# Kernel optimization log

Hardware: AMD Instinct MI355X
Metric: run time of the kernel (lower is better)

The kernel has to match this reference:

```python
import jax, jax.numpy as jnp
import numpy as np

HID, H, D, DFF = 128, 4, 128, 2048   # hidden_dim, nheads, out_feats per head, dim_feedforward
N, E, B = 32768, 524288, 32
EPS = 1e-5
SLOPE = 0.2  # DGL EdgeGATConv negative_slope default


def setup_inputs() -> dict:
    key = jax.random.key(0)
    ks = jax.random.split(key, 16)
    s = 0.05
    return {
        "h": jax.random.normal(ks[0], (N, HID), jnp.float32),
        "e": jax.random.normal(ks[1], (E, 1), jnp.float32),
        "src": jax.random.randint(ks[2], (E,), 0, N, jnp.int32),
        "dst": jax.random.randint(ks[3], (E,), 0, N, jnp.int32),
        "batch_size": B,
        # EdgeGATConv params (fc / fc_edge / res_fc are bias-free in DGL)
        "W_fc": jax.random.normal(ks[4], (HID, H * D), jnp.float32) * s,
        "attn_l": jax.random.normal(ks[5], (H, D), jnp.float32) * s,
        "attn_r": jax.random.normal(ks[6], (H, D), jnp.float32) * s,
        "W_fe": jax.random.normal(ks[7], (1, H * D), jnp.float32) * s,
        "attn_e": jax.random.normal(ks[8], (H, D), jnp.float32) * s,
        "W_res": jax.random.normal(ks[9], (HID, H * D), jnp.float32) * s,
        "gat_bias": jnp.zeros((H * D,), jnp.float32),
        # linear_mha + norms + FFN
        "W_mha": jax.random.normal(ks[10], (H * D, HID), jnp.float32) * s,
        "b_mha": jnp.zeros((HID,), jnp.float32),
        "n1_g": jnp.ones((HID,), jnp.float32),
        "n1_b": jnp.zeros((HID,), jnp.float32),
        "n2_g": jnp.ones((HID,), jnp.float32),
        "n2_b": jnp.zeros((HID,), jnp.float32),
        "W1": jax.random.normal(ks[11], (HID, DFF), jnp.float32) * s,
        "b1": jnp.zeros((DFF,), jnp.float32),
        "W2": jax.random.normal(ks[12], (DFF, HID), jnp.float32) * s,
        "b2": jnp.zeros((HID,), jnp.float32),
    }


def _ln(x, g, b):
    mu = x.mean(-1, keepdims=True)
    var = ((x - mu) ** 2).mean(-1, keepdims=True)
    return (x - mu) * jax.lax.rsqrt(var + EPS) * g + b


def reference(h, e, src, dst, batch_size, W_fc, attn_l, attn_r, W_fe, attn_e,
              W_res, gat_bias, W_mha, b_mha, n1_g, n1_b, n2_g, n2_b,
              W1, b1, W2, b2):
    n = h.shape[0]
    h0 = h
    # --- EdgeGATConv (eval mode: dropouts are identity) ---
    ft = (h @ W_fc).reshape(n, H, D)                         # (N,H,D)
    el = jnp.einsum("nhd,hd->nh", ft, attn_l)                # (N,H)
    er = jnp.einsum("nhd,hd->nh", ft, attn_r)
    fe = (e @ W_fe).reshape(-1, H, D)                        # (E,H,D)
    ee = jnp.einsum("ehd,hd->eh", fe, attn_e)                # (E,H)
    sc = jax.nn.leaky_relu(el[src] + er[dst] + ee, SLOPE)    # (E,H)
    # segment softmax over incoming edges of each dst node
    m = jax.ops.segment_max(sc, dst, num_segments=n)         # (N,H)
    m = jnp.where(jnp.isfinite(m), m, 0.0)                   # empty segments
    w = jnp.exp(sc - m[dst])
    z = jax.ops.segment_sum(w, dst, num_segments=n)
    zd = z[dst]
    alpha = w / jnp.where(zd == 0, 1.0, zd)                  # (E,H)
    msg = ft[src] * alpha[:, :, None]                        # (E,H,D)
    rst = jax.ops.segment_sum(msg, dst, num_segments=n)      # (N,H,D)
    rst = rst + (h0 @ W_res).reshape(n, H, D) + gat_bias.reshape(1, H, D)
    # --- transformer wrapper ---
    x = jax.nn.relu(rst).reshape(n, H * D)
    x = jax.nn.relu(x @ W_mha + b_mha)
    x = _ln(h0 + x, n1_g, n1_b)
    x = x.reshape(batch_size, -1, x.shape[1])                # (B, N/B, HID)
    ff = jax.nn.relu(x @ W1 + b1) @ W2 + b2
    return _ln(x + ff, n2_g, n2_b)
```

## Files before the change

kernel.cpp:

```cpp
#include <hip/hip_runtime.h>
#include <hip/hip_bf16.h>

#define N_NODES 32768
#define E_EDGES 524288
#define HIDDIM 128
#define FDIM 512
#define DFF 2048
#define LN_EPS 1e-5f
#define SLOPE 0.2f
#define CAP 64

typedef __bf16 bf16_t;
typedef __bf16 bf16x8 __attribute__((ext_vector_type(8)));
typedef float f32x4 __attribute__((ext_vector_type(4)));
typedef float f32x2 __attribute__((ext_vector_type(2)));

#define GLD_LDS16(gp, lp) __builtin_amdgcn_global_load_lds( \
    (const __attribute__((address_space(1))) unsigned int*)(gp), \
    (__attribute__((address_space(3))) unsigned int*)(lp), 16, 0, 0)

__device__ inline unsigned char f32_to_e4m3(float v) {
#if __has_builtin(__builtin_amdgcn_cvt_pk_fp8_f32)
    return (unsigned char)(__builtin_amdgcn_cvt_pk_fp8_f32(v, v, 0, false) & 0xff);
#else
    unsigned bits = __float_as_uint(v);
    unsigned sign = (bits >> 24) & 0x80;
    float av = fabsf(v);
    if (av >= 448.f) return (unsigned char)(sign | 0x7E);
    int e = (int)((bits >> 23) & 0xFF) - 127;
    if (e < -6) { int n = (int)rintf(av * 512.f); return (unsigned char)(sign | n); }
    float ulp = exp2f((float)(e - 3));
    int n = (int)rintf(av / ulp);
    if (n == 16) { e += 1; n = 8; }
    return (unsigned char)(sign | ((e + 7) << 3) | (n - 8));
#endif
}
template<bool HI>
__device__ inline f32x2 e4m3x2_to_f32(unsigned u) {
#if __has_builtin(__builtin_amdgcn_cvt_pk_f32_fp8)
    return __builtin_amdgcn_cvt_pk_f32_fp8(u, HI);
#else
    f32x2 r;
    unsigned b0 = HI ? ((u >> 16) & 0xff) : (u & 0xff);
    unsigned b1 = HI ? ((u >> 24) & 0xff) : ((u >> 8) & 0xff);
    unsigned bs[2] = {b0, b1};
    for (int i = 0; i < 2; ++i) {
        unsigned b = bs[i];
        float s = (b & 0x80) ? -1.f : 1.f;
        int e = (b >> 3) & 15, m = b & 7;
        float v = e ? (8 + m) * exp2f((float)(e - 10)) : m * exp2f(-9.f);
        r[i] = s * v;
    }
    return r;
#endif
}

__device__ inline void pack_range(const float* __restrict__ B, bf16_t* __restrict__ out,
                                  int id, int N) {
    const int g = id / N, n = id % N;
    union { bf16_t b[8]; uint4 u; } pk;
#pragma unroll
    for (int j = 0; j < 8; ++j) pk.b[j] = (bf16_t)B[(size_t)(g * 8 + j) * N + n];
    *(uint4*)(out + (size_t)id * 8) = pk.u;
}

__global__ __launch_bounds__(256) void prep_kernel(const float* __restrict__ h, bf16_t* __restrict__ hb,
                                                   const float* __restrict__ W_fc, bf16_t* __restrict__ Wfc_p,
                                                   const float* __restrict__ W_res, bf16_t* __restrict__ Wres_p,
                                                   const float* __restrict__ W_mha, bf16_t* __restrict__ Wmha_p,
                                                   const float* __restrict__ W1, bf16_t* __restrict__ W1_p,
                                                   const float* __restrict__ W2, bf16_t* __restrict__ W2_p,
                                                   const float* __restrict__ W_fe, const float* __restrict__ attn_e,
                                                   float* __restrict__ ce) {
    int bid = blockIdx.x;
    const int tid = threadIdx.x;
    if (bid < 4096) {
        const int id = bid * 256 + tid;
        const float4 v = ((const float4*)h)[id];
        union { bf16_t b[4]; uint2 u; } pk;
        pk.b[0] = (bf16_t)v.x; pk.b[1] = (bf16_t)v.y; pk.b[2] = (bf16_t)v.z; pk.b[3] = (bf16_t)v.w;
        *(uint2*)(hb + (size_t)id * 4) = pk.u;
        return;
    }
    bid -= 4096;
    if (bid < 32)  { pack_range(W_fc,  Wfc_p,  bid * 256 + tid, 512);  return; }
    bid -= 32;
    if (bid < 32)  { pack_range(W_res, Wres_p, bid * 256 + tid, 512);  return; }
    bid -= 32;
    if (bid < 32)  { pack_range(W_mha, Wmha_p, bid * 256 + tid, 128);  return; }
    bid -= 32;
    if (bid < 128) { pack_range(W1,    W1_p,   bid * 256 + tid, 2048); return; }
    bid -= 128;
    if (bid < 128) { pack_range(W2,    W2_p,   bid * 256 + tid, 128);  return; }
    if (tid < 128) {
        const float4 w = ((const float4*)W_fe)[tid];
        const float4 a = ((const float4*)attn_e)[tid];
        float p = w.x * a.x + w.y * a.y + w.z * a.z + w.w * a.w;
        for (int off = 16; off; off >>= 1) p += __shfl_down(p, off, 32);
        if ((tid & 31) == 0) ce[tid >> 5] = p;
    }
}

__global__ __launch_bounds__(256) void gemm_mfma(const bf16_t* __restrict__ A,
                                                 const bf16_t* __restrict__ Bp,
                                                 bf16_t* __restrict__ C,
                                                 int M, int N, int K) {
    __shared__ __align__(16) bf16_t lA[4096];
    __shared__ __align__(16) bf16_t lB[4096];
    const int tid = threadIdx.x;
    const int lane = tid & 63;
    const int wave = tid >> 6;
    const int wm = (wave >> 1) * 64, wn = (wave & 1) * 64;
    const int row0 = blockIdx.y * 128, col0 = blockIdx.x * 128;
    const int ko = lane >> 4;
    const int rl = lane & 15;
    f32x4 acc[4][4] = {};
    const int c0 = tid, c1 = tid + 256;
    const int g0 = c0 >> 7, m0 = c0 & 127;
    const int g1 = c1 >> 7, m1 = c1 & 127;
    for (int k0 = 0; k0 < K; k0 += 32) {
        __syncthreads();
        GLD_LDS16(A + (size_t)(row0 + m0) * K + k0 + g0 * 8, lA + c0 * 8);
        GLD_LDS16(A + (size_t)(row0 + m1) * K + k0 + g1 * 8, lA + c1 * 8);
        GLD_LDS16(Bp + ((size_t)(k0 / 8 + g0) * N + col0 + m0) * 8, lB + c0 * 8);
        GLD_LDS16(Bp + ((size_t)(k0 / 8 + g1) * N + col0 + m1) * 8, lB + c1 * 8);
        __syncthreads();
        bf16x8 af[4], bfr[4];
#pragma unroll
        for (int i = 0; i < 4; ++i) {
            af[i]  = *(const bf16x8*)&lA[(ko * 128 + wm + i * 16 + rl) * 8];
            bfr[i] = *(const bf16x8*)&lB[(ko * 128 + wn + i * 16 + rl) * 8];
        }
#pragma unroll
        for (int i = 0; i < 4; ++i)
#pragma unroll
            for (int j = 0; j < 4; ++j)
                acc[i][j] = __builtin_amdgcn_mfma_f32_16x16x32_bf16(af[i], bfr[j], acc[i][j], 0, 0, 0);
    }
    const int cr = (lane >> 4) * 4;
    const int cc = lane & 15;
#pragma unroll
    for (int i = 0; i < 4; ++i)
#pragma unroll
        for (int j = 0; j < 4; ++j) {
            const int col = col0 + wn + j * 16 + cc;
#pragma unroll
            for (int r = 0; r < 4; ++r) {
                const int row = row0 + wm + i * 16 + cr + r;
                C[(size_t)row * N + col] = (bf16_t)acc[i][j][r];
            }
        }
}

__global__ __launch_bounds__(256) void gemm_ft(const bf16_t* __restrict__ A,
                                               const bf16_t* __restrict__ Bp,
                                               const float* __restrict__ attn_l,
                                               const float* __restrict__ attn_r,
                                               unsigned char* __restrict__ ft8,
                                               float* __restrict__ el,
                                               float* __restrict__ er) {
    __shared__ __align__(16) bf16_t lA[4096];
    __shared__ __align__(16) bf16_t lB[4096];
    __shared__ float s_el[2][128], s_er[2][128];
    const int tid = threadIdx.x, lane = tid & 63, wave = tid >> 6;
    const int wm = (wave >> 1) * 64, wn = (wave & 1) * 64;
    const int row0 = blockIdx.y * 128;
    const int head = blockIdx.x, col0 = head * 128;
    const int ko = lane >> 4, rl = lane & 15;
    f32x4 acc[4][4] = {};
    const int c0 = tid, c1 = tid + 256;
    const int g0 = c0 >> 7, m0 = c0 & 127;
    const int g1 = c1 >> 7, m1 = c1 & 127;
    for (int k0 = 0; k0 < 128; k0 += 32) {
        __syncthreads();
        GLD_LDS16(A + (size_t)(row0 + m0) * 128 + k0 + g0 * 8, lA + c0 * 8);
        GLD_LDS16(A + (size_t)(row0 + m1) * 128 + k0 + g1 * 8, lA + c1 * 8);
        GLD_LDS16(Bp + ((size_t)(k0 / 8 + g0) * 512 + col0 + m0) * 8, lB + c0 * 8);
        GLD_LDS16(Bp + ((size_t)(k0 / 8 + g1) * 512 + col0 + m1) * 8, lB + c1 * 8);
        __syncthreads();
        bf16x8 af[4], bfr[4];
#pragma unroll
        for (int i = 0; i < 4; ++i) {
            af[i]  = *(const bf16x8*)&lA[(ko * 128 + wm + i * 16 + rl) * 8];
            bfr[i] = *(const bf16x8*)&lB[(ko * 128 + wn + i * 16 + rl) * 8];
        }
#pragma unroll
        for (int i = 0; i < 4; ++i)
#pragma unroll
            for (int j = 0; j < 4; ++j)
                acc[i][j] = __builtin_amdgcn_mfma_f32_16x16x32_bf16(af[i], bfr[j], acc[i][j], 0, 0, 0);
    }
    const int cr = (lane >> 4) * 4, cc = lane & 15;
    float al[4], ar[4];
#pragma unroll
    for (int j = 0; j < 4; ++j) {
        al[j] = attn_l[col0 + wn + j * 16 + cc];
        ar[j] = attn_r[col0 + wn + j * 16 + cc];
    }
#pragma unroll
    for (int i = 0; i < 4; ++i)
#pragma unroll
        for (int r = 0; r < 4; ++r) {
            const int row = row0 + wm + i * 16 + cr + r;
            float pel = 0.f, per = 0.f;
#pragma unroll
            for (int j = 0; j < 4; ++j) {
                const float v = acc[i][j][r];
                ft8[(size_t)row * 512 + col0 + wn + j * 16 + cc] = f32_to_e4m3(v);
                pel += v * al[j];
                per += v * ar[j];
            }
#pragma unroll
            for (int m = 1; m < 16; m <<= 1) {
                pel += __shfl_xor(pel, m);
                per += __shfl_xor(per, m);
            }
            if (cc == 0) {
                s_el[wn >> 6][wm + i * 16 + cr + r] = pel;
                s_er[wn >> 6][wm + i * 16 + cr + r] = per;
            }
        }
    __syncthreads();
    if (tid < 128) {
        el[(size_t)(row0 + tid) * 4 + head] = s_el[0][tid] + s_el[1][tid];
        er[(size_t)(row0 + tid) * 4 + head] = s_er[0][tid] + s_er[1][tid];
    }
}

__global__ __launch_bounds__(256) void gemm_mha_ln(const bf16_t* __restrict__ A,
                                                   const bf16_t* __restrict__ Bp,
                                                   const float* __restrict__ bias,
                                                   const float* __restrict__ h0,
                                                   const float* __restrict__ gamma,
                                                   const float* __restrict__ beta,
                                                   bf16_t* __restrict__ out) {
    __shared__ __align__(16) bf16_t lA[4096];
    __shared__ __align__(16) bf16_t lB[4096];
    __shared__ float s_s1[2][128], s_s2[2][128], s_mu[128], s_rs[128];
    const int tid = threadIdx.x, lane = tid & 63, wave = tid >> 6;
    const int wm = (wave >> 1) * 64, wn = (wave & 1) * 64;
    const int row0 = blockIdx.x * 128;
    const int ko = lane >> 4, rl = lane & 15;
    f32x4 acc[4][4] = {};
    const int c0 = tid, c1 = tid + 256;
    const int g0 = c0 >> 7, m0 = c0 & 127;
    const int g1 = c1 >> 7, m1 = c1 & 127;
    for (int k0 = 0; k0 < 512; k0 += 32) {
        __syncthreads();
        GLD_LDS16(A + (size_t)(row0 + m0) * 512 + k0 + g0 * 8, lA + c0 * 8);
        GLD_LDS16(A + (size_t)(row0 + m1) * 512 + k0 + g1 * 8, lA + c1 * 8);
        GLD_LDS16(Bp + ((size_t)(k0 / 8 + g0) * 128 + m0) * 8, lB + c0 * 8);
        GLD_LDS16(Bp + ((size_t)(k0 / 8 + g1) * 128 + m1) * 8, lB + c1 * 8);
        __syncthreads();
        bf16x8 af[4], bfr[4];
#pragma unroll
        for (int i = 0; i < 4; ++i) {
            af[i]  = *(const bf16x8*)&lA[(ko * 128 + wm + i * 16 + rl) * 8];
            bfr[i] = *(const bf16x8*)&lB[(ko * 128 + wn + i * 16 + rl) * 8];
        }
#pragma unroll
        for (int i = 0; i < 4; ++i)
#pragma unroll
            for (int j = 0; j < 4; ++j)
                acc[i][j] = __builtin_amdgcn_mfma_f32_16x16x32_bf16(af[i], bfr[j], acc[i][j], 0, 0, 0);
    }
    const int cr = (lane >> 4) * 4, cc = lane & 15;
#pragma unroll
    for (int j = 0; j < 4; ++j) {
        const int col = wn + j * 16 + cc;
        const float bb = bias[col];
#pragma unroll
        for (int i = 0; i < 4; ++i)
#pragma unroll
            for (int r = 0; r < 4; ++r) {
                const int row = row0 + wm + i * 16 + cr + r;
                acc[i][j][r] = fmaxf(acc[i][j][r] + bb, 0.f) + h0[(size_t)row * 128 + col];
            }
    }
#pragma unroll
    for (int i = 0; i < 4; ++i)
#pragma unroll
        for (int r = 0; r < 4; ++r) {
            float s1 = 0.f, s2 = 0.f;
#pragma unroll
            for (int j = 0; j < 4; ++j) { const float v = acc[i][j][r]; s1 += v; s2 += v * v; }
#pragma unroll
            for (int m = 1; m < 16; m <<= 1) {
                s1 += __shfl_xor(s1, m);
                s2 += __shfl_xor(s2, m);
            }
            if (cc == 0) {
                s_s1[wn >> 6][wm + i * 16 + cr + r] = s1;
                s_s2[wn >> 6][wm + i * 16 + cr + r] = s2;
            }
        }
    __syncthreads();
    if (tid < 128) {
        const float a = s_s1[0][tid] + s_s1[1][tid];
        const float q = s_s2[0][tid] + s_s2[1][tid];
        const float mu = a * (1.f / 128.f);
        s_mu[tid] = mu;
        s_rs[tid] = rsqrtf(q * (1.f / 128.f) - mu * mu + LN_EPS);
    }
    __syncthreads();
#pragma unroll
    for (int j = 0; j < 4; ++j) {
        const int col = wn + j * 16 + cc;
        const float gg = gamma[col], bb = beta[col];
#pragma unroll
        for (int i = 0; i < 4; ++i)
#pragma unroll
            for (int r = 0; r < 4; ++r) {
                const int rloc = wm + i * 16 + cr + r;
                out[(size_t)(row0 + rloc) * 128 + col] =
                    (bf16_t)((acc[i][j][r] - s_mu[rloc]) * s_rs[rloc] * gg + bb);
            }
    }
}

__global__ __launch_bounds__(256, 1) void ffn_fused(const bf16_t* __restrict__ x3,
                                                    const bf16_t* __restrict__ W1p,
                                                    const float* __restrict__ b1,
                                                    const bf16_t* __restrict__ W2p,
                                                    const float* __restrict__ b2,
                                                    const float* __restrict__ gamma,
                                                    const float* __restrict__ beta,
                                                    float* __restrict__ out) {
    __shared__ __align__(16) bf16_t lX[16384];
    __shared__ __align__(16) bf16_t lW1[2][8192];
    __shared__ __align__(16) bf16_t lW2[2][8192];
    __shared__ __align__(16) bf16_t lY[8192];
    __shared__ float s_s1[2][128], s_s2[2][128], s_mu[128], s_rs[128];
    const int tid = threadIdx.x, lane = tid & 63, wave = tid >> 6;
    const int wm = (wave >> 1) * 64;
    const int wn1 = (wave & 1) * 32;
    const int wn2 = (wave & 1) * 64;
    const int row0 = blockIdx.x * 128;
    const int ko = lane >> 4, rl = lane & 15;
    const int cr = ko * 4, cc = rl;

#pragma unroll
    for (int it = 0; it < 8; ++it) {
        const int c = it * 256 + tid, g = c >> 7, m = c & 127;
        GLD_LDS16(x3 + (size_t)(row0 + m) * 128 + g * 8, lX + c * 8);
    }
#pragma unroll
    for (int it = 0; it < 4; ++it) {
        const int c = it * 256 + tid;
        { const int g = c >> 6, n = c & 63;  GLD_LDS16(W1p + ((size_t)g * 2048 + n) * 8, lW1[0] + c * 8); }
        { const int g = c >> 7, n = c & 127; GLD_LDS16(W2p + ((size_t)g * 128 + n) * 8, lW2[0] + c * 8); }
    }
    __syncthreads();
    bf16x8 afx[4][4];
#pragma unroll
    for (int i = 0; i < 4; ++i)
#pragma unroll
        for (int kk = 0; kk < 4; ++kk)
            afx[i][kk] = *(const bf16x8*)&lX[((kk * 4 + ko) * 128 + wm + i * 16 + rl) * 8];

    f32x4 xacc[4][4] = {};
    for (int ch = 0; ch < 32; ++ch) {
        const int b = ch & 1;
        f32x4 yacc[4][2] = {};
#pragma unroll
        for (int kk = 0; kk < 4; ++kk) {
            bf16x8 bfr[2];
#pragma unroll
            for (int j = 0; j < 2; ++j)
                bfr[j] = *(const bf16x8*)&lW1[b][((kk * 4 + ko) * 64 + wn1 + j * 16 + rl) * 8];
#pragma unroll
            for (int i = 0; i < 4; ++i)
#pragma unroll
                for (int j = 0; j < 2; ++j)
                    yacc[i][j] = __builtin_amdgcn_mfma_f32_16x16x32_bf16(afx[i][kk], bfr[j], yacc[i][j], 0, 0, 0);
        }
#pragma unroll
        for (int j = 0; j < 2; ++j) {
            const int dff = wn1 + j * 16 + cc;
            const float bb = b1[ch * 64 + dff];
#pragma unroll
            for (int i = 0; i < 4; ++i)
#pragma unroll
                for (int r = 0; r < 4; ++r)
                    lY[((dff >> 3) * 128 + wm + i * 16 + cr + r) * 8 + (dff & 7)] =
                        (bf16_t)fmaxf(yacc[i][j][r] + bb, 0.f);
        }
        __syncthreads();
        if (ch + 1 < 32) {
            const int nb = b ^ 1, nch = ch + 1;
#pragma unroll
            for (int it = 0; it < 4; ++it) {
                const int c = it * 256 + tid;
                { const int g = c >> 6, n = c & 63;  GLD_LDS16(W1p + ((size_t)g * 2048 + nch * 64 + n) * 8, lW1[nb] + c * 8); }
                { const int g = c >> 7, n = c & 127; GLD_LDS16(W2p + ((size_t)(nch * 8 + g) * 128 + n) * 8, lW2[nb] + c * 8); }
            }
        }
#pragma unroll
        for (int kk = 0; kk < 2; ++kk) {
            bf16x8 afY[4], bfr2[4];
#pragma unroll
            for (int i = 0; i < 4; ++i)
                afY[i] = *(const bf16x8*)&lY[((kk * 4 + ko) * 128 + wm + i * 16 + rl) * 8];
#pragma unroll
            for (int j = 0; j < 4; ++j)
                bfr2[j] = *(const bf16x8*)&lW2[b][((kk * 4 + ko) * 128 + wn2 + j * 16 + rl) * 8];
#pragma unroll
            for (int i = 0; i < 4; ++i)
#pragma unroll
                for (int j = 0; j < 4; ++j)
                    xacc[i][j] = __builtin_amdgcn_mfma_f32_16x16x32_bf16(afY[i], bfr2[j], xacc[i][j], 0, 0, 0);
        }
        __syncthreads();
    }
#pragma unroll
    for (int j = 0; j < 4; ++j) {
        const int col = wn2 + j * 16 + cc;
        const float bb = b2[col];
#pragma unroll
        for (int i = 0; i < 4; ++i)
#pragma unroll
            for (int r = 0; r < 4; ++r) {
                const int rloc = wm + i * 16 + cr + r;
                const float x3v = (float)lX[((col >> 3) * 128 + rloc) * 8 + (col & 7)];
                xacc[i][j][r] += bb + x3v;
            }
    }
#pragma unroll
    for (int i = 0; i < 4; ++i)
#pragma unroll
        for (int r = 0; r < 4; ++r) {
            float s1 = 0.f, s2 = 0.f;
#pragma unroll
            for (int j = 0; j < 4; ++j) { const float v = xacc[i][j][r]; s1 += v; s2 += v * v; }
#pragma unroll
            for (int m = 1; m < 16; m <<= 1) {
                s1 += __shfl_xor(s1, m);
                s2 += __shfl_xor(s2, m);
            }
            if (cc == 0) {
                s_s1[wn2 >> 6][wm + i * 16 + cr + r] = s1;
                s_s2[wn2 >> 6][wm + i * 16 + cr + r] = s2;
            }
        }
    __syncthreads();
    if (tid < 128) {
        const float a = s_s1[0][tid] + s_s1[1][tid];
        const float q = s_s2[0][tid] + s_s2[1][tid];
        const float mu = a * (1.f / 128.f);
        s_mu[tid] = mu;
        s_rs[tid] = rsqrtf(q * (1.f / 128.f) - mu * mu + LN_EPS);
    }
    __syncthreads();
#pragma unroll
    for (int j = 0; j < 4; ++j) {
        const int col = wn2 + j * 16 + cc;
        const float gg = gamma[col], bb = beta[col];
#pragma unroll
        for (int i = 0; i < 4; ++i)
#pragma unroll
            for (int r = 0; r < 4; ++r) {
                const int rloc = wm + i * 16 + cr + r;
                out[(size_t)(row0 + rloc) * 128 + col] =
                    (xacc[i][j][r] - s_mu[rloc]) * s_rs[rloc] * gg + bb;
            }
    }
}

__global__ __launch_bounds__(256) void edge_build(const float* __restrict__ evals,
                                                  const int* __restrict__ src,
                                                  const int* __restrict__ dst,
                                                  const float* __restrict__ el,
                                                  const float* __restrict__ er,
                                                  const float* __restrict__ ce,
                                                  int* __restrict__ cursor,
                                                  int* __restrict__ csr_src,
                                                  float4* __restrict__ csr_w) {
    const int e = blockIdx.x * 256 + threadIdx.x;
    const int s = src[e], d = dst[e];
    const float ev = evals[e];
    const float4 l = *(const float4*)(el + (size_t)s * 4);
    const float4 r = *(const float4*)(er + (size_t)d * 4);
    const float4 c = *(const float4*)ce;
    float4 w;
    {
        float v;
        v = l.x + r.x + ev * c.x; v = v >= 0.f ? v : SLOPE * v; w.x = __expf(v);
        v = l.y + r.y + ev * c.y; v = v >= 0.f ? v : SLOPE * v; w.y = __expf(v);
        v = l.z + r.z + ev * c.z; v = v >= 0.f ? v : SLOPE * v; w.z = __expf(v);
        v = l.w + r.w + ev * c.w; v = v >= 0.f ? v : SLOPE * v; w.w = __expf(v);
    }
    const int pos = atomicAdd(&cursor[d], 1);
    if (pos < CAP) {
        csr_src[(size_t)d * CAP + pos] = s;
        csr_w[(size_t)d * CAP + pos] = w;
    }
}

__global__ __launch_bounds__(128) void aggregate_kernel(const unsigned char* __restrict__ ft8,
                                                        const bf16_t* __restrict__ res,
                                                        const int* __restrict__ cursor,
                                                        const int* __restrict__ csr_src,
                                                        const float4* __restrict__ csr_w,
                                                        const float* __restrict__ gat_bias,
                                                        bf16_t* __restrict__ x1) {
    const int n = blockIdx.x, t = threadIdx.x;
    __shared__ int s_src[CAP];
    __shared__ float s_w[CAP][4];
    const int deg = min(cursor[n], CAP);
    const int ht = t >> 5;
    if (t < deg) {
        s_src[t] = csr_src[(size_t)n * CAP + t];
        *(float4*)s_w[t] = csr_w[(size_t)n * CAP + t];
    }
    __syncthreads();
    float4 acc = {0.f, 0.f, 0.f, 0.f};
    float z = 0.f;
    for (int j = 0; j < deg; ++j) {
        const float w = s_w[j][ht];
        z += w;
        const unsigned u = *(const unsigned*)(ft8 + (size_t)s_src[j] * 512 + t * 4);
        const f32x2 lo = e4m3x2_to_f32<false>(u);
        const f32x2 hi = e4m3x2_to_f32<true>(u);
        acc.x += w * lo[0]; acc.y += w * lo[1];
        acc.z += w * hi[0]; acc.w += w * hi[1];
    }
    const float rz = deg > 0 ? 1.f / z : 0.f;
    const uint2 ur = *(const uint2*)(res + (size_t)n * FDIM + t * 4);
    const float4 gb = ((const float4*)gat_bias)[t];
    union { bf16_t b[4]; uint2 u; } pk;
    pk.b[0] = (bf16_t)fmaxf(acc.x * rz + __uint_as_float(ur.x << 16) + gb.x, 0.f);
    pk.b[1] = (bf16_t)fmaxf(acc.y * rz + __uint_as_float(ur.x & 0xFFFF0000u) + gb.y, 0.f);
    pk.b[2] = (bf16_t)fmaxf(acc.z * rz + __uint_as_float(ur.y << 16) + gb.z, 0.f);
    pk.b[3] = (bf16_t)fmaxf(acc.w * rz + __uint_as_float(ur.y & 0xFFFF0000u) + gb.w, 0.f);
    *(uint2*)(x1 + (size_t)n * FDIM + t * 4) = pk.u;
}

extern "C" void kernel_launch(void* const* d_in, const int* in_sizes, int n_in,
                              void* d_out, int out_size, void* d_ws, size_t ws_size,
                              hipStream_t stream) {
    const float* h        = (const float*)d_in[0];
    const float* evals    = (const float*)d_in[1];
    const int*   src      = (const int*)d_in[2];
    const int*   dst      = (const int*)d_in[3];
    const float* W_fc     = (const float*)d_in[5];
    const float* attn_l   = (const float*)d_in[6];
    const float* attn_r   = (const float*)d_in[7];
    const float* W_fe     = (const float*)d_in[8];
    const float* attn_e   = (const float*)d_in[9];
    const float* W_res    = (const float*)d_in[10];
    const float* gat_bias = (const float*)d_in[11];
    const float* W_mha    = (const float*)d_in[12];
    const float* b_mha    = (const float*)d_in[13];
    const float* n1_g     = (const float*)d_in[14];
    const float* n1_b     = (const float*)d_in[15];
    const float* n2_g     = (const float*)d_in[16];
    const float* n2_b     = (const float*)d_in[17];
    const float* W1       = (const float*)d_in[18];
    const float* b1       = (const float*)d_in[19];
    const float* W2       = (const float*)d_in[20];
    const float* b2       = (const float*)d_in[21];

    char* ws = (char*)d_ws;
    unsigned char* ft8 = (unsigned char*)(ws + 0);
    bf16_t* res     = (bf16_t*)(ws + 16777216ull);
    bf16_t* x1      = (bf16_t*)(ws + 50331648ull);
    float4* csr_w   = (float4*)(ws + 83886080ull);
    int*    csr_src = (int*)   (ws + 117440512ull);
    bf16_t* x3b     = (bf16_t*)(ws + 125829120ull);
    bf16_t* hb      = (bf16_t*)(ws + 134217728ull);
    bf16_t* Wfc_p   = (bf16_t*)(ws + 142606336ull);
    bf16_t* Wres_p  = (bf16_t*)(ws + 142737408ull);
    bf16_t* Wmha_p  = (bf16_t*)(ws + 142868480ull);
    bf16_t* W1_p    = (bf16_t*)(ws + 142999552ull);
    bf16_t* W2_p    = (bf16_t*)(ws + 143523840ull);
    float*  el      = (float*) (ws + 144048128ull);
    float*  er      = (float*) (ws + 144572416ull);
    float*  ce      = (float*) (ws + 145096704ull);
    int*    cursor  = (int*)   (ws + 145096768ull);

    if (ws_size < 146000000ull) return;

    (void)hipMemsetAsync(cursor, 0, 131072, stream);

    prep_kernel<<<4449, 256, 0, stream>>>(h, hb, W_fc, Wfc_p, W_res, Wres_p,
                                          W_mha, Wmha_p, W1, W1_p, W2, W2_p,
                                          W_fe, attn_e, ce);
    gemm_ft<<<dim3(4, 256), 256, 0, stream>>>(hb, Wfc_p, attn_l, attn_r, ft8, el, er);
    gemm_mfma<<<dim3(4, 256), 256, 0, stream>>>(hb, Wres_p, res, N_NODES, FDIM, 128);
    edge_build<<<E_EDGES / 256, 256, 0, stream>>>(evals, src, dst, el, er, ce, cursor, csr_src, csr_w);
    aggregate_kernel<<<N_NODES, 128, 0, stream>>>(ft8, res, cursor, csr_src, csr_w, gat_bias, x1);
    gemm_mha_ln<<<256, 256, 0, stream>>>(x1, Wmha_p, b_mha, h, n1_g, n1_b, x3b);
    ffn_fused<<<256, 256, 0, stream>>>(x3b, W1_p, b1, W2_p, b2, n2_g, n2_b, (float*)d_out);
}
```

Baseline: 328.7 us.

## Halve FFN row tile to 64 and drop weight double-buffering for more blocks

The fused FFN kernel now processes 64 rows per block instead of 128, launching 512 blocks with launch bounds allowing two blocks per CU. The double-buffered W1/W2 LDS staging and the persistent X tile in LDS are removed, which shrinks LDS and register use. The aim is to fill all CUs (256 CUs with 512 blocks) and raise occupancy. In exchange, each weight chunk is loaded synchronously with no prefetch overlap, weight traffic per row doubles, and the residual is re-read from global memory.

Measured after the change: 297.7 us. 1.1x faster.

```diff
diff --git a/kernel.cpp b/kernel.cpp
--- a/kernel.cpp
+++ b/kernel.cpp
@@ -318,7 +318,7 @@
     }
 }
 
-__global__ __launch_bounds__(256, 1) void ffn_fused(const bf16_t* __restrict__ x3,
+__global__ __launch_bounds__(256, 2) void ffn_fused(const bf16_t* __restrict__ x3,
                                                     const bf16_t* __restrict__ W1p,
                                                     const float* __restrict__ b1,
                                                     const bf16_t* __restrict__ W2p,
@@ -326,107 +326,96 @@
                                                     const float* __restrict__ gamma,
                                                     const float* __restrict__ beta,
                                                     float* __restrict__ out) {
-    __shared__ __align__(16) bf16_t lX[16384];
-    __shared__ __align__(16) bf16_t lW1[2][8192];
-    __shared__ __align__(16) bf16_t lW2[2][8192];
-    __shared__ __align__(16) bf16_t lY[8192];
-    __shared__ float s_s1[2][128], s_s2[2][128], s_mu[128], s_rs[128];
+    __shared__ __align__(16) bf16_t lW1[8192];
+    __shared__ __align__(16) bf16_t lW2[8192];
+    __shared__ __align__(16) bf16_t lY[4096];
+    __shared__ float s_s1[2][64], s_s2[2][64], s_mu[64], s_rs[64];
     const int tid = threadIdx.x, lane = tid & 63, wave = tid >> 6;
-    const int wm = (wave >> 1) * 64;
-    const int wn1 = (wave & 1) * 32;
-    const int wn2 = (wave & 1) * 64;
-    const int row0 = blockIdx.x * 128;
+    const int wr  = (wave >> 1) * 32;
+    const int wc1 = (wave & 1) * 32;
+    const int wc2 = (wave & 1) * 64;
+    const int row0 = blockIdx.x * 64;
     const int ko = lane >> 4, rl = lane & 15;
     const int cr = ko * 4, cc = rl;
 
 #pragma unroll
-    for (int it = 0; it < 8; ++it) {
-        const int c = it * 256 + tid, g = c >> 7, m = c & 127;
-        GLD_LDS16(x3 + (size_t)(row0 + m) * 128 + g * 8, lX + c * 8);
-    }
-#pragma unroll
     for (int it = 0; it < 4; ++it) {
-        const int c = it * 256 + tid;
-        { const int g = c >> 6, n = c & 63;  GLD_LDS16(W1p + ((size_t)g * 2048 + n) * 8, lW1[0] + c * 8); }
-        { const int g = c >> 7, n = c & 127; GLD_LDS16(W2p + ((size_t)g * 128 + n) * 8, lW2[0] + c * 8); }
-    }
-    __syncthreads();
-    bf16x8 afx[4][4];
-#pragma unroll
-    for (int i = 0; i < 4; ++i)
+        const int c = it * 256 + tid, g = c >> 6, m = c & 63;
+        GLD_LDS16(x3 + (size_t)(row0 + m) * 128 + g * 8, lW1 + c * 8);
+    }
+    __syncthreads();
+    bf16x8 afx[2][4];
+#pragma unroll
+    for (int i = 0; i < 2; ++i)
 #pragma unroll
         for (int kk = 0; kk < 4; ++kk)
-            afx[i][kk] = *(const bf16x8*)&lX[((kk * 4 + ko) * 128 + wm + i * 16 + rl) * 8];
-
-    f32x4 xacc[4][4] = {};
+            afx[i][kk] = *(const bf16x8*)&lW1[((kk * 4 + ko) * 64 + wr + i * 16 + rl) * 8];
+
+    f32x4 xacc[2][4] = {};
     for (int ch = 0; ch < 32; ++ch) {
-        const int b = ch & 1;
-        f32x4 yacc[4][2] = {};
+        __syncthreads();
+#pragma unroll
+        for (int it = 0; it < 4; ++it) {
+            const int c = it * 256 + tid;
+            { const int g = c >> 6, n = c & 63;  GLD_LDS16(W1p + ((size_t)g * 2048 + ch * 64 + n) * 8, lW1 + c * 8); }
+            { const int g = c >> 7, n = c & 127; GLD_LDS16(W2p + ((size_t)(ch * 8 + g) * 128 + n) * 8, lW2 + c * 8); }
+        }
+        __syncthreads();
+        f32x4 yacc[2][2] = {};
 #pragma unroll
         for (int kk = 0; kk < 4; ++kk) {
             bf16x8 bfr[2];
 #pragma unroll
             for (int j = 0; j < 2; ++j)
-                bfr[j] = *(const bf16x8*)&lW1[b][((kk * 4 + ko) * 64 + wn1 + j * 16 + rl) * 8];
-#pragma unroll
-            for (int i = 0; i < 4; ++i)
+                bfr[j] = *(const bf16x8*)&lW1[((kk * 4 + ko) * 64 + wc1 + j * 16 + rl) * 8];
+#pragma unroll
+            for (int i = 0; i < 2; ++i)
 #pragma unroll
                 for (int j = 0; j < 2; ++j)
                     yacc[i][j] = __builtin_amdgcn_mfma_f32_16x16x32_bf16(afx[i][kk], bfr[j], yacc[i][j], 0, 0, 0);
         }
 #pragma unroll
         for (int j = 0; j < 2; ++j) {
-            const int dff = wn1 + j * 16 + cc;
+            const int dff = wc1 + j * 16 + cc;
             const float bb = b1[ch * 64 + dff];
 #pragma unroll
-            for (int i = 0; i < 4; ++i)
+            for (int i = 0; i < 2; ++i)
 #pragma unroll
                 for (int r = 0; r < 4; ++r)
-                    lY[((dff >> 3) * 128 + wm + i * 16 + cr + r) * 8 + (dff & 7)] =
+                    lY[((dff >> 3) * 64 + wr + i * 16 + cr + r) * 8 + (dff & 7)] =
                         (bf16_t)fmaxf(yacc[i][j][r] + bb, 0.f);
         }
         __syncthreads();
-        if (ch + 1 < 32) {
-            const int nb = b ^ 1, nch = ch + 1;
-#pragma unroll
-            for (int it = 0; it < 4; ++it) {
-                const int c = it * 256 + tid;
-                { const int g = c >> 6, n = c & 63;  GLD_LDS16(W1p + ((size_t)g * 2048 + nch * 64 + n) * 8, lW1[nb] + c * 8); }
-                { const int g = c >> 7, n = c & 127; GLD_LDS16(W2p + ((size_t)(nch * 8 + g) * 128 + n) * 8, lW2[nb] + c * 8); }
-            }
-        }
 #pragma unroll
         for (int kk = 0; kk < 2; ++kk) {
-            bf16x8 afY[4], bfr2[4];
-#pragma unroll
-            for (int i = 0; i < 4; ++i)
-                afY[i] = *(const bf16x8*)&lY[((kk * 4 + ko) * 128 + wm + i * 16 + rl) * 8];
+            bf16x8 afY[2], bfr2[4];
+#pragma unroll
+            for (int i = 0; i < 2; ++i)
+                afY[i] = *(const bf16x8*)&lY[((kk * 4 + ko) * 64 + wr + i * 16 + rl) * 8];
 #pragma unroll
             for (int j = 0; j < 4; ++j)
-                bfr2[j] = *(const bf16x8*)&lW2[b][((kk * 4 + ko) * 128 + wn2 + j * 16 + rl) * 8];
-#pragma unroll
-            for (int i = 0; i < 4; ++i)
+                bfr2[j] = *(const bf16x8*)&lW2[((kk * 4 + ko) * 128 + wc2 + j * 16 + rl) * 8];
+#pragma unroll
+            for (int i = 0; i < 2; ++i)
 #pragma unroll
                 for (int j = 0; j < 4; ++j)
                     xacc[i][j] = __builtin_amdgcn_mfma_f32_16x16x32_bf16(afY[i], bfr2[j], xacc[i][j], 0, 0, 0);
         }
-        __syncthreads();
     }
 #pragma unroll
     for (int j = 0; j < 4; ++j) {
-        const int col = wn2 + j * 16 + cc;
+        const int col = wc2 + j * 16 + cc;
         const float bb = b2[col];
 #pragma unroll
-        for (int i = 0; i < 4; ++i)
+        for (int i = 0; i < 2; ++i)
 #pragma unroll
             for (int r = 0; r < 4; ++r) {
-                const int rloc = wm + i * 16 + cr + r;
-                const float x3v = (float)lX[((col >> 3) * 128 + rloc) * 8 + (col & 7)];
-                xacc[i][j][r] += bb + x3v;
-            }
-    }
-#pragma unroll
-    for (int i = 0; i < 4; ++i)
+                const int row = wr + i * 16 + cr + r;
+                xacc[i][j][r] += bb + (float)x3[(size_t)(row0 + row) * 128 + col];
+            }
+    }
+#pragma unroll
+    for (int i = 0; i < 2; ++i)
 #pragma unroll
         for (int r = 0; r < 4; ++r) {
             float s1 = 0.f, s2 = 0.f;
@@ -438,12 +427,12 @@
                 s2 += __shfl_xor(s2, m);
             }
             if (cc == 0) {
-                s_s1[wn2 >> 6][wm + i * 16 + cr + r] = s1;
-                s_s2[wn2 >> 6][wm + i * 16 + cr + r] = s2;
-            }
-        }
-    __syncthreads();
-    if (tid < 128) {
+                s_s1[wave & 1][wr + i * 16 + cr + r] = s1;
+                s_s2[wave & 1][wr + i * 16 + cr + r] = s2;
+            }
+        }
+    __syncthreads();
+    if (tid < 64) {
         const float a = s_s1[0][tid] + s_s1[1][tid];
         const float q = s_s2[0][tid] + s_s2[1][tid];
         const float mu = a * (1.f / 128.f);
@@ -453,13 +442,13 @@
     __syncthreads();
 #pragma unroll
     for (int j = 0; j < 4; ++j) {
-        const int col = wn2 + j * 16 + cc;
+        const int col = wc2 + j * 16 + cc;
         const float gg = gamma[col], bb = beta[col];
 #pragma unroll
-        for (int i = 0; i < 4; ++i)
+        for (int i = 0; i < 2; ++i)
 #pragma unroll
             for (int r = 0; r < 4; ++r) {
-                const int rloc = wm + i * 16 + cr + r;
+                const int rloc = wr + i * 16 + cr + r;
                 out[(size_t)(row0 + rloc) * 128 + col] =
                     (xacc[i][j][r] - s_mu[rloc]) * s_rs[rloc] * gg + bb;
             }
@@ -590,5 +579,5 @@
     edge_build<<<E_EDGES / 256, 256, 0, stream>>>(evals, src, dst, el, er, ce, cursor, csr_src, csr_w);
     aggregate_kernel<<<N_NODES, 128, 0, stream>>>(ft8, res, cursor, csr_src, csr_w, gat_bias, x1);
     gemm_mha_ln<<<256, 256, 0, stream>>>(x1, Wmha_p, b_mha, h, n1_g, n1_b, x3b);
-    ffn_fused<<<256, 256, 0, stream>>>(x3b, W1_p, b1, W2_p, b2, n2_g, n2_b, (float*)d_out);
-}
+    ffn_fused<<<512, 256, 0, stream>>>(x3b, W1_p, b1, W2_p, b2, n2_g, n2_b, (float*)d_out);
+}
```

## Repartition FFN waves by rows so each wave owns full output rows

Applied to the files above, without the earlier changes.

The fused FFN kernel now gives each of the four waves 32 full rows and all output columns, instead of a 2x2 split over rows and columns. This removes the LDS staging of the input tile, one of the two barriers per DFF chunk, and the cross-wave shared-memory reduction for the final LayerNorm, since each wave can normalise its own rows with shuffles. The input fragments are read straight from global memory into registers, and the weight prefetch is issued before the first GEMM. In exchange every wave must read all weight columns from LDS, which roughly doubles LDS weight traffic per wave, and the residual and parameter reads in the epilogue now go to global memory.

After: 323.7 us. Within noise of the previous version (-1.5%).

```diff
diff --git a/kernel.cpp b/kernel.cpp
--- a/kernel.cpp
+++ b/kernel.cpp
@@ -326,66 +326,32 @@
                                                     const float* __restrict__ gamma,
                                                     const float* __restrict__ beta,
                                                     float* __restrict__ out) {
-    __shared__ __align__(16) bf16_t lX[16384];
     __shared__ __align__(16) bf16_t lW1[2][8192];
     __shared__ __align__(16) bf16_t lW2[2][8192];
     __shared__ __align__(16) bf16_t lY[8192];
-    __shared__ float s_s1[2][128], s_s2[2][128], s_mu[128], s_rs[128];
     const int tid = threadIdx.x, lane = tid & 63, wave = tid >> 6;
-    const int wm = (wave >> 1) * 64;
-    const int wn1 = (wave & 1) * 32;
-    const int wn2 = (wave & 1) * 64;
+    const int wr = wave * 32;
     const int row0 = blockIdx.x * 128;
     const int ko = lane >> 4, rl = lane & 15;
     const int cr = ko * 4, cc = rl;
 
-#pragma unroll
-    for (int it = 0; it < 8; ++it) {
-        const int c = it * 256 + tid, g = c >> 7, m = c & 127;
-        GLD_LDS16(x3 + (size_t)(row0 + m) * 128 + g * 8, lX + c * 8);
-    }
 #pragma unroll
     for (int it = 0; it < 4; ++it) {
         const int c = it * 256 + tid;
         { const int g = c >> 6, n = c & 63;  GLD_LDS16(W1p + ((size_t)g * 2048 + n) * 8, lW1[0] + c * 8); }
         { const int g = c >> 7, n = c & 127; GLD_LDS16(W2p + ((size_t)g * 128 + n) * 8, lW2[0] + c * 8); }
     }
+    bf16x8 afx[2][4];
+#pragma unroll
+    for (int i = 0; i < 2; ++i)
+#pragma unroll
+        for (int kk = 0; kk < 4; ++kk)
+            afx[i][kk] = *(const bf16x8*)&x3[(size_t)(row0 + wr + i * 16 + rl) * 128 + (kk * 4 + ko) * 8];
     __syncthreads();
-    bf16x8 afx[4][4];
-#pragma unroll
-    for (int i = 0; i < 4; ++i)
-#pragma unroll
-        for (int kk = 0; kk < 4; ++kk)
-            afx[i][kk] = *(const bf16x8*)&lX[((kk * 4 + ko) * 128 + wm + i * 16 + rl) * 8];
-
-    f32x4 xacc[4][4] = {};
+
+    f32x4 xacc[2][8] = {};
     for (int ch = 0; ch < 32; ++ch) {
         const int b = ch & 1;
-        f32x4 yacc[4][2] = {};
-#pragma unroll
-        for (int kk = 0; kk < 4; ++kk) {
-            bf16x8 bfr[2];
-#pragma unroll
-            for (int j = 0; j < 2; ++j)
-                bfr[j] = *(const bf16x8*)&lW1[b][((kk * 4 + ko) * 64 + wn1 + j * 16 + rl) * 8];
-#pragma unroll
-            for (int i = 0; i < 4; ++i)
-#pragma unroll
-                for (int j = 0; j < 2; ++j)
-                    yacc[i][j] = __builtin_amdgcn_mfma_f32_16x16x32_bf16(afx[i][kk], bfr[j], yacc[i][j], 0, 0, 0);
-        }
-#pragma unroll
-        for (int j = 0; j < 2; ++j) {
-            const int dff = wn1 + j * 16 + cc;
-            const float bb = b1[ch * 64 + dff];
-#pragma unroll
-            for (int i = 0; i < 4; ++i)
-#pragma unroll
-                for (int r = 0; r < 4; ++r)
-                    lY[((dff >> 3) * 128 + wm + i * 16 + cr + r) * 8 + (dff & 7)] =
-                        (bf16_t)fmaxf(yacc[i][j][r] + bb, 0.f);
-        }
-        __syncthreads();
         if (ch + 1 < 32) {
             const int nb = b ^ 1, nch = ch + 1;
 #pragma unroll
@@ -395,75 +361,73 @@
                 { const int g = c >> 7, n = c & 127; GLD_LDS16(W2p + ((size_t)(nch * 8 + g) * 128 + n) * 8, lW2[nb] + c * 8); }
             }
         }
+        f32x4 yacc[2][4] = {};
+#pragma unroll
+        for (int kk = 0; kk < 4; ++kk) {
+            bf16x8 bfr[4];
+#pragma unroll
+            for (int j = 0; j < 4; ++j)
+                bfr[j] = *(const bf16x8*)&lW1[b][((kk * 4 + ko) * 64 + j * 16 + rl) * 8];
+#pragma unroll
+            for (int i = 0; i < 2; ++i)
+#pragma unroll
+                for (int j = 0; j < 4; ++j)
+                    yacc[i][j] = __builtin_amdgcn_mfma_f32_16x16x32_bf16(afx[i][kk], bfr[j], yacc[i][j], 0, 0, 0);
+        }
+#pragma unroll
+        for (int j = 0; j < 4; ++j) {
+            const int dff = j * 16 + cc;
+            const float bb = b1[ch * 64 + dff];
+#pragma unroll
+            for (int i = 0; i < 2; ++i)
+#pragma unroll
+                for (int r = 0; r < 4; ++r)
+                    lY[((dff >> 3) * 128 + wr + i * 16 + cr + r) * 8 + (dff & 7)] =
+                        (bf16_t)fmaxf(yacc[i][j][r] + bb, 0.f);
+        }
 #pragma unroll
         for (int kk = 0; kk < 2; ++kk) {
-            bf16x8 afY[4], bfr2[4];
-#pragma unroll
-            for (int i = 0; i < 4; ++i)
-                afY[i] = *(const bf16x8*)&lY[((kk * 4 + ko) * 128 + wm + i * 16 + rl) * 8];
-#pragma unroll
-            for (int j = 0; j < 4; ++j)
-                bfr2[j] = *(const bf16x8*)&lW2[b][((kk * 4 + ko) * 128 + wn2 + j * 16 + rl) * 8];
-#pragma unroll
-            for (int i = 0; i < 4; ++i)
-#pragma unroll
-                for (int j = 0; j < 4; ++j)
-                    xacc[i][j] = __builtin_amdgcn_mfma_f32_16x16x32_bf16(afY[i], bfr2[j], xacc[i][j], 0, 0, 0);
-        }
-        __syncthreads();
-    }
-#pragma unroll
-    for (int j = 0; j < 4; ++j) {
-        const int col = wn2 + j * 16 + cc;
-        const float bb = b2[col];
-#pragma unroll
-        for (int i = 0; i < 4; ++i)
-#pragma unroll
-            for (int r = 0; r < 4; ++r) {
-                const int rloc = wm + i * 16 + cr + r;
-                const float x3v = (float)lX[((col >> 3) * 128 + rloc) * 8 + (col & 7)];
-                xacc[i][j][r] += bb + x3v;
-            }
-    }
-#pragma unroll
-    for (int i = 0; i < 4; ++i)
+            bf16x8 afY[2];
+#pragma unroll
+            for (int i = 0; i < 2; ++i)
+                afY[i] = *(const bf16x8*)&lY[((kk * 4 + ko) * 128 + wr + i * 16 + rl) * 8];
+#pragma unroll
+            for (int j = 0; j < 8; ++j) {
+                const bf16x8 bfr2 = *(const bf16x8*)&lW2[b][((kk * 4 + ko) * 128 + j * 16 + rl) * 8];
+#pragma unroll
+                for (int i = 0; i < 2; ++i)
+                    xacc[i][j] = __builtin_amdgcn_mfma_f32_16x16x32_bf16(afY[i], bfr2, xacc[i][j], 0, 0, 0);
+            }
+        }
+        __syncthreads();
+    }
+#pragma unroll
+    for (int i = 0; i < 2; ++i)
 #pragma unroll
         for (int r = 0; r < 4; ++r) {
+            const int row = wr + i * 16 + cr + r;
             float s1 = 0.f, s2 = 0.f;
 #pragma unroll
-            for (int j = 0; j < 4; ++j) { const float v = xacc[i][j][r]; s1 += v; s2 += v * v; }
+            for (int j = 0; j < 8; ++j) {
+                const int col = j * 16 + cc;
+                float v = xacc[i][j][r] + b2[col] + (float)x3[(size_t)(row0 + row) * 128 + col];
+                xacc[i][j][r] = v;
+                s1 += v; s2 += v * v;
+            }
 #pragma unroll
             for (int m = 1; m < 16; m <<= 1) {
                 s1 += __shfl_xor(s1, m);
                 s2 += __shfl_xor(s2, m);
             }
-            if (cc == 0) {
-                s_s1[wn2 >> 6][wm + i * 16 + cr + r] = s1;
-                s_s2[wn2 >> 6][wm + i * 16 + cr + r] = s2;
-            }
-        }
-    __syncthreads();
-    if (tid < 128) {
-        const float a = s_s1[0][tid] + s_s1[1][tid];
-        const float q = s_s2[0][tid] + s_s2[1][tid];
-        const float mu = a * (1.f / 128.f);
-        s_mu[tid] = mu;
-        s_rs[tid] = rsqrtf(q * (1.f / 128.f) - mu * mu + LN_EPS);
-    }
-    __syncthreads();
-#pragma unroll
-    for (int j = 0; j < 4; ++j) {
-        const int col = wn2 + j * 16 + cc;
-        const float gg = gamma[col], bb = beta[col];
-#pragma unroll
-        for (int i = 0; i < 4; ++i)
-#pragma unroll
-            for (int r = 0; r < 4; ++r) {
-                const int rloc = wm + i * 16 + cr + r;
-                out[(size_t)(row0 + rloc) * 128 + col] =
-                    (xacc[i][j][r] - s_mu[rloc]) * s_rs[rloc] * gg + bb;
-            }
-    }
+            const float mu = s1 * (1.f / 128.f);
+            const float rs = rsqrtf(s2 * (1.f / 128.f) - mu * mu + LN_EPS);
+#pragma unroll
+            for (int j = 0; j < 8; ++j) {
+                const int col = j * 16 + cc;
+                out[(size_t)(row0 + row) * 128 + col] =
+                    (xacc[i][j][r] - mu) * rs * gamma[col] + beta[col];
+            }
+        }
 }
 
 __global__ __launch_bounds__(256) void edge_build(const float* __restrict__ evals,
```
